# Kernel tuning notes

Measured on AMD Instinct MI355X. Metric: run time of the kernel, lower is better.

Reference implementation:

```python
import jax, jax.numpy as jnp
import numpy as np

S, B, E, H, V, L = 512, 64, 512, 768, 32000, 32
PAD_WORD, PAD_LABEL = 1, 0
PAD_BIAS = 10000.0


def _linear_init(key, fin, fout):
    # matches torch nn.Linear default U(-1/sqrt(fin), 1/sqrt(fin))
    kw, kb = jax.random.split(key)
    s = 1.0 / np.sqrt(fin)
    W = jax.random.uniform(kw, (fin, fout), minval=-s, maxval=s, dtype=jnp.float32)
    b = jax.random.uniform(kb, (fout,), minval=-s, maxval=s, dtype=jnp.float32)
    return W, b


def setup_inputs() -> dict:
    key = jax.random.key(0)
    ks = jax.random.split(key, 9)
    tokens = jax.random.randint(ks[0], (S, B), 0, V, dtype=jnp.int32)
    tags = jax.random.randint(ks[1], (S, B), 0, L, dtype=jnp.int32)
    embedding = jax.random.normal(ks[2], (V, E), dtype=jnp.float32)
    # gate order along the 4H axis: r, f, g, o (matches the 8 separate Linears, stacked)
    Wi_f, bi_f = _linear_init(ks[3], E, 4 * H)
    Wh_f, bh_f = _linear_init(ks[4], H, 4 * H)
    Wi_b, bi_b = _linear_init(ks[5], E, 4 * H)
    Wh_b, bh_b = _linear_init(ks[6], H, 4 * H)
    Wout, bout = _linear_init(ks[7], 2 * H, L)
    return {"tokens": tokens, "tags": tags, "embedding": embedding,
            "Wi_f": Wi_f, "bi_f": bi_f, "Wh_f": Wh_f, "bh_f": bh_f,
            "Wi_b": Wi_b, "bi_b": bi_b, "Wh_b": Wh_b, "bh_b": bh_b,
            "Wout": Wout, "bout": bout}


def _forward(tokens, embedding, Wi_f, bi_f, Wh_f, bh_f, Wi_b, bi_b, Wh_b, bh_b, Wout, bout):
    emb = embedding[tokens]                      # [S,B,E]
    b = tokens.shape[1]
    h = emb.shape[-1] * 0 + Wh_f.shape[0]
    # ---- forward direction: true LSTM-style recurrence ----
    xf = jnp.einsum('sbe,eg->sbg', emb, Wi_f) + bi_f   # [S,B,4H] precomputed input gates

    def step_f(carry, x):
        hid, c = carry
        g = x + hid @ Wh_f + bh_f
        r, f, gg, o = jnp.split(g, 4, axis=-1)
        c = jax.nn.sigmoid(f) * c + jax.nn.sigmoid(r) * jnp.tanh(gg)
        hid = jax.nn.sigmoid(o) * jnp.tanh(c)
        return (hid, c), hid

    z = jnp.zeros((b, h), dtype=emb.dtype)
    (hT, _), hs_f = jax.lax.scan(step_f, (z, z), xf)   # hs_f: [S,B,H]

    # ---- backward direction: source never updates `hidden`, so the hidden
    # projection uses the CONSTANT final forward hidden hT at every step.
    gb = jnp.einsum('sbe,eg->sbg', emb, Wi_b) + bi_b + hT @ Wh_b + bh_b  # [S,B,4H]
    r2, f2, g2, o2 = jnp.split(gb, 4, axis=-1)
    r2 = jax.nn.sigmoid(r2); f2 = jax.nn.sigmoid(f2)
    g2 = jnp.tanh(g2);       o2 = jax.nn.sigmoid(o2)

    def step_b(c2, gates):
        r, f, g, o = gates
        c2 = f * c2 + r * g
        return c2, o * jnp.tanh(c2)

    _, hs_b = jax.lax.scan(step_b, z, (r2, f2, g2, o2), reverse=True)  # [S,B,H], original order

    outputs = jnp.concatenate([hs_f, hs_b], axis=-1)   # [S,B,2H]
    out = outputs @ Wout + bout                        # [S,B,L]
    pad_mask = (tokens == PAD_WORD).astype(out.dtype)
    out = out.at[:, :, PAD_LABEL].add(pad_mask * PAD_BIAS)
    return out


def reference(tokens, tags, embedding, Wi_f, bi_f, Wh_f, bh_f, Wi_b, bi_b, Wh_b, bh_b, Wout, bout):
    del tags  # unused in forward, kept for signature fidelity
    return _forward(tokens, embedding, Wi_f, bi_f, Wh_f, bh_f, Wi_b, bi_b, Wh_b, bh_b, Wout, bout)
```

## Files before the change

kernel.cpp:

```cpp
#include <hip/hip_runtime.h>
#include <hip/hip_bf16.h>
#include <stdint.h>

typedef __attribute__((ext_vector_type(8))) short bf16x8;
typedef __attribute__((ext_vector_type(4))) float f32x4;
typedef __attribute__((ext_vector_type(4))) unsigned int u32x4;
typedef unsigned long long ull_t;

#define S_LEN 512
#define B_DIM 64
#define E_DIM 512
#define H_DIM 768
#define G4    3072
#define H2    1536
#define M_ROWS 32768
#define CHUNK 128
#define CM    8192
#define SLW   24
#define WPS   8
#define WPR   256
#define RWRD  4096
#define PSTR  16384
#define KRES  640
#define KREG  4
#define WROW  648
#define NTILES 1536

__device__ __forceinline__ float sigmf_(float x) { return 1.0f / (1.0f + __expf(-x)); }
__device__ __forceinline__ float tanhf2(float x) {
  x = fminf(fmaxf(x, -20.0f), 20.0f);
  float e = __expf(2.0f * x);
  return (e - 1.0f) / (e + 1.0f);
}
__device__ __forceinline__ float bfu(unsigned short u) { return __uint_as_float((unsigned)u << 16); }
__device__ __forceinline__ unsigned short packbf(float a) {
  __hip_bfloat16 t = __float2bfloat16(a);
  unsigned short b;
  __builtin_memcpy(&b, &t, 2);
  return b;
}

__global__ __launch_bounds__(256) void k_gather(const int* __restrict__ tokens,
                                                const float* __restrict__ emb,
                                                __hip_bfloat16* __restrict__ out) {
  const int t = blockIdx.x * 256 + threadIdx.x;
  const int e0 = t * 8;
  const int row = e0 >> 9;
  const int k = e0 & 511;
  const int tok = tokens[row];
  const float4* p = (const float4*)(emb + (size_t)tok * E_DIM + k);
  const float4 v0 = p[0], v1 = p[1];
  __align__(16) __hip_bfloat16 tmp[8];
  tmp[0] = __float2bfloat16(v0.x); tmp[1] = __float2bfloat16(v0.y);
  tmp[2] = __float2bfloat16(v0.z); tmp[3] = __float2bfloat16(v0.w);
  tmp[4] = __float2bfloat16(v1.x); tmp[5] = __float2bfloat16(v1.y);
  tmp[6] = __float2bfloat16(v1.z); tmp[7] = __float2bfloat16(v1.w);
  *(bf16x8*)(out + (size_t)t * 8) = *(const bf16x8*)tmp;
}

__global__ __launch_bounds__(256) void k_transpose_cast(const float* __restrict__ src,
                                                        __hip_bfloat16* __restrict__ dst,
                                                        int Rs, int Cs) {
  __shared__ float tile[32][33];
  const int tx = threadIdx.x & 31, ty = threadIdx.x >> 5;
  const int c0 = blockIdx.x * 32, r0 = blockIdx.y * 32;
  #pragma unroll
  for (int i = ty; i < 32; i += 8)
    tile[i][tx] = src[(size_t)(r0 + i) * Cs + c0 + tx];
  __syncthreads();
  #pragma unroll
  for (int i = ty; i < 32; i += 8)
    dst[(size_t)(c0 + i) * Rs + r0 + tx] = __float2bfloat16(tile[tx][i]);
}

__global__ __launch_bounds__(256) void k_bias(const float* __restrict__ bi,
                                              const float* __restrict__ bh,
                                              float* __restrict__ bias) {
  const int n = blockIdx.x * 256 + threadIdx.x;
  bias[n] = bi[n] + bh[n];
}

__device__ __forceinline__ void gemm_tile_e(char* pool, int tile,
                                            const __hip_bfloat16* __restrict__ A,
                                            const __hip_bfloat16* __restrict__ BT,
                                            const float* __restrict__ bias,
                                            __hip_bfloat16* __restrict__ C) {
  auto As = (__hip_bfloat16 (*)[40])pool;
  auto Bs = (__hip_bfloat16 (*)[40])(pool + 10240);
  const int tid = threadIdx.x;
  const int wave = tid >> 6, lane = tid & 63;
  const int q = lane >> 4, lr = lane & 15;
  const int wm = (wave >> 1) * 64, wn = (wave & 1) * 64;
  const int nb = tile % 24, mb = tile / 24;
  const int m0 = mb * 128, n0 = nb * 128;
  const int srow = tid >> 2, skseg = (tid & 3) * 8;

  f32x4 acc[4][4];
  #pragma unroll
  for (int i = 0; i < 4; ++i)
    #pragma unroll
    for (int j = 0; j < 4; ++j) { f32x4 z = {0.f, 0.f, 0.f, 0.f}; acc[i][j] = z; }

  for (int kt = 0; kt < 16; ++kt) {
    __syncthreads();
    const int kbase = kt * 32 + skseg;
    *(bf16x8*)&As[srow][skseg]      = *(const bf16x8*)(A + (size_t)(m0 + srow) * E_DIM + kbase);
    *(bf16x8*)&As[srow + 64][skseg] = *(const bf16x8*)(A + (size_t)(m0 + srow + 64) * E_DIM + kbase);
    *(bf16x8*)&Bs[srow][skseg]      = *(const bf16x8*)(BT + (size_t)(n0 + srow) * E_DIM + kbase);
    *(bf16x8*)&Bs[srow + 64][skseg] = *(const bf16x8*)(BT + (size_t)(n0 + srow + 64) * E_DIM + kbase);
    __syncthreads();
    bf16x8 af[4], bfr[4];
    #pragma unroll
    for (int mt = 0; mt < 4; ++mt) af[mt] = *(const bf16x8*)&As[wm + mt * 16 + lr][q * 8];
    #pragma unroll
    for (int nt = 0; nt < 4; ++nt) bfr[nt] = *(const bf16x8*)&Bs[wn + nt * 16 + lr][q * 8];
    #pragma unroll
    for (int mt = 0; mt < 4; ++mt)
      #pragma unroll
      for (int nt = 0; nt < 4; ++nt)
        acc[mt][nt] = __builtin_amdgcn_mfma_f32_16x16x32_bf16(af[mt], bfr[nt], acc[mt][nt], 0, 0, 0);
  }
  #pragma unroll
  for (int mt = 0; mt < 4; ++mt) {
    #pragma unroll
    for (int nt = 0; nt < 4; ++nt) {
      const int col = n0 + wn + nt * 16 + lr;
      const float bv = bias[col];
      #pragma unroll
      for (int i = 0; i < 4; ++i) {
        const int row = m0 + wm + mt * 16 + q * 4 + i;
        C[(size_t)row * G4 + col] = __float2bfloat16(acc[mt][nt][i] + bv);
      }
    }
  }
}

__device__ __forceinline__ void gemm_tile_g(char* pool, int tile,
                                            const int* __restrict__ tokens_c,
                                            const float* __restrict__ emb,
                                            const __hip_bfloat16* __restrict__ BT,
                                            const float* __restrict__ bias,
                                            __hip_bfloat16* __restrict__ C) {
  auto As = (__hip_bfloat16 (*)[40])pool;
  auto Bs = (__hip_bfloat16 (*)[40])(pool + 10240);
  const int tid = threadIdx.x;
  const int wave = tid >> 6, lane = tid & 63;
  const int q = lane >> 4, lr = lane & 15;
  const int wm = (wave >> 1) * 64, wn = (wave & 1) * 64;
  const int nb = tile % 24, mb = tile / 24;
  const int m0 = mb * 128, n0 = nb * 128;
  const int srow = tid >> 2, skseg = (tid & 3) * 8;
  const int tok0 = tokens_c[m0 + srow];
  const int tok1 = tokens_c[m0 + srow + 64];

  f32x4 acc[4][4];
  #pragma unroll
  for (int i = 0; i < 4; ++i)
    #pragma unroll
    for (int j = 0; j < 4; ++j) { f32x4 z = {0.f, 0.f, 0.f, 0.f}; acc[i][j] = z; }

  for (int kt = 0; kt < 16; ++kt) {
    __syncthreads();
    const int kbase = kt * 32 + skseg;
    {
      const float* ap = emb + (size_t)tok0 * E_DIM + kbase;
      const float4 v0 = *(const float4*)ap, v1 = *(const float4*)(ap + 4);
      __align__(16) __hip_bfloat16 t8[8];
      t8[0] = __float2bfloat16(v0.x); t8[1] = __float2bfloat16(v0.y);
      t8[2] = __float2bfloat16(v0.z); t8[3] = __float2bfloat16(v0.w);
      t8[4] = __float2bfloat16(v1.x); t8[5] = __float2bfloat16(v1.y);
      t8[6] = __float2bfloat16(v1.z); t8[7] = __float2bfloat16(v1.w);
      *(bf16x8*)&As[srow][skseg] = *(const bf16x8*)t8;
    }
    {
      const float* ap = emb + (size_t)tok1 * E_DIM + kbase;
      const float4 v0 = *(const float4*)ap, v1 = *(const float4*)(ap + 4);
      __align__(16) __hip_bfloat16 t8[8];
      t8[0] = __float2bfloat16(v0.x); t8[1] = __float2bfloat16(v0.y);
      t8[2] = __float2bfloat16(v0.z); t8[3] = __float2bfloat16(v0.w);
      t8[4] = __float2bfloat16(v1.x); t8[5] = __float2bfloat16(v1.y);
      t8[6] = __float2bfloat16(v1.z); t8[7] = __float2bfloat16(v1.w);
      *(bf16x8*)&As[srow + 64][skseg] = *(const bf16x8*)t8;
    }
    *(bf16x8*)&Bs[srow][skseg]      = *(const bf16x8*)(BT + (size_t)(n0 + srow) * E_DIM + kbase);
    *(bf16x8*)&Bs[srow + 64][skseg] = *(const bf16x8*)(BT + (size_t)(n0 + srow + 64) * E_DIM + kbase);
    __syncthreads();
    bf16x8 af[4], bfr[4];
    #pragma unroll
    for (int mt = 0; mt < 4; ++mt) af[mt] = *(const bf16x8*)&As[wm + mt * 16 + lr][q * 8];
    #pragma unroll
    for (int nt = 0; nt < 4; ++nt) bfr[nt] = *(const bf16x8*)&Bs[wn + nt * 16 + lr][q * 8];
    #pragma unroll
    for (int mt = 0; mt < 4; ++mt)
      #pragma unroll
      for (int nt = 0; nt < 4; ++nt)
        acc[mt][nt] = __builtin_amdgcn_mfma_f32_16x16x32_bf16(af[mt], bfr[nt], acc[mt][nt], 0, 0, 0);
  }
  #pragma unroll
  for (int mt = 0; mt < 4; ++mt) {
    #pragma unroll
    for (int nt = 0; nt < 4; ++nt) {
      const int col = n0 + wn + nt * 16 + lr;
      const float bv = bias[col];
      #pragma unroll
      for (int i = 0; i < 4; ++i) {
        const int row = m0 + wm + mt * 16 + q * 4 + i;
        C[(size_t)row * G4 + col] = __float2bfloat16(acc[mt][nt][i] + bv);
      }
    }
  }
}

__global__ __launch_bounds__(256) void k_gemm_e(const __hip_bfloat16* __restrict__ A,
                                                const __hip_bfloat16* __restrict__ BT,
                                                const float* __restrict__ bias,
                                                __hip_bfloat16* __restrict__ C) {
  __shared__ __align__(16) char pool[20480];
  gemm_tile_e(pool, blockIdx.x, A, BT, bias, C);
}
__global__ __launch_bounds__(256) void k_gemm_g(const int* __restrict__ tokens_c,
                                                const float* __restrict__ emb,
                                                const __hip_bfloat16* __restrict__ BT,
                                                const float* __restrict__ bias,
                                                __hip_bfloat16* __restrict__ C) {
  __shared__ __align__(16) char pool[20480];
  gemm_tile_g(pool, blockIdx.x, tokens_c, emb, BT, bias, C);
}

__device__ __forceinline__ void out_block8(char* pool, int ob,
                                           const __hip_bfloat16* __restrict__ Hs,
                                           const float* __restrict__ Wout,
                                           const float* __restrict__ bout,
                                           const int* __restrict__ tokens,
                                           float* __restrict__ out) {
  auto rowbuf = (float (*)[1536])pool;
  const int r0 = ob * 8;
  const int tid = threadIdx.x;
  for (int idx = tid; idx < 8 * 1536; idx += 256) {
    const int rr = idx / 1536, k = idx % 1536;
    rowbuf[rr][k] = __bfloat162float(Hs[(size_t)(r0 + rr) * H2 + k]);
  }
  __syncthreads();
  const int l = tid & 31, rr = tid >> 5;
  float acc = bout[l];
  #pragma unroll 8
  for (int k = 0; k < 1536; ++k) acc += rowbuf[rr][k] * Wout[k * 32 + l];
  const int row = r0 + rr;
  if (l == 0 && tokens[row] == 1) acc += 10000.0f;
  out[(size_t)row * 32 + l] = acc;
  __syncthreads();
}

__global__ __launch_bounds__(256) void k_out(const __hip_bfloat16* __restrict__ Hs,
                                             const float* __restrict__ Wout,
                                             const float* __restrict__ bout,
                                             const int* __restrict__ tokens,
                                             float* __restrict__ out) {
  __shared__ __align__(16) char pool[49152];
  out_block8(pool, blockIdx.x, Hs, Wout, bout, tokens, out);
}

__global__ __launch_bounds__(256, 1) void k_fwd_fused(const __hip_bfloat16* __restrict__ X,
                                                      const __hip_bfloat16* __restrict__ WhTf,
                                                      ull_t* __restrict__ hbuf,
                                                      __hip_bfloat16* __restrict__ Hs,
                                                      float* __restrict__ cstate,
                                                      float* __restrict__ hT,
                                                      int chunk,
                                                      const __hip_bfloat16* __restrict__ EmbA,
                                                      const int* __restrict__ tokens_nx,
                                                      const float* __restrict__ emb,
                                                      const __hip_bfloat16* __restrict__ WiT_nx,
                                                      const float* __restrict__ Bias_nx,
                                                      __hip_bfloat16* __restrict__ Xw) {
  __shared__ __align__(16) char pool[155904];
  const int bx = blockIdx.x;

  if (bx >= 128) {
    const int nw = gridDim.x - 128;
    if (EmbA) {
      for (int t = bx - 128; t < NTILES; t += nw)
        gemm_tile_e(pool, t, EmbA, WiT_nx, Bias_nx, Xw);
    } else {
      for (int t = bx - 128; t < NTILES; t += nw)
        gemm_tile_g(pool, t, tokens_nx, emb, WiT_nx, Bias_nx, Xw);
    }
    return;
  }

  unsigned short* wlds = (unsigned short*)pool;
  auto h_stage = (unsigned short (*)[776])(pool + 124416);
  auto g_lds   = (float (*)[16][26])(pool + 149248);

  const int group = bx >> 5;
  const int slice = bx & 31;
  const int r0 = group * 16;
  const int j0 = slice * SLW;
  const int tid = threadIdx.x;
  const int w = tid >> 6;
  const int lane = tid & 63;
  const int q = lane >> 4, lr = lane & 15;
  const int base = chunk * CHUNK;

  const int prow = tid >> 4;
  const int pw   = tid & 15;

  const int row  = tid >> 3;
  const int wloc = tid & 7;
  const int col0 = 3 * wloc;

  for (int c = tid; c < 96 * (KRES / 8); c += 256) {
    const int r = c / (KRES / 8), k8 = c % (KRES / 8);
    const int gate = r / SLW, n = r % SLW;
    const float4 v = *(const float4*)(WhTf + (size_t)(gate * H_DIM + j0 + n) * H_DIM + k8 * 8);
    *(float4*)(wlds + (size_t)r * WROW + k8 * 8) = v;
  }

  const int wn0 = lr;
  const int wn1 = 16 + (lr & 7);
  bf16x8 wr0[KREG], wr1[KREG];
  #pragma unroll
  for (int kk = 0; kk < KREG; ++kk) {
    const int ko = KRES + kk * 32 + q * 8;
    wr0[kk] = *(const bf16x8*)(WhTf + (size_t)(w * H_DIM + j0 + wn0) * H_DIM + ko);
    wr1[kk] = *(const bf16x8*)(WhTf + (size_t)(w * H_DIM + j0 + wn1) * H_DIM + ko);
  }

  float cr[3] = {0.f, 0.f, 0.f};
  if (tid < 128) {
    const float* cs = cstate + (size_t)(r0 + row) * H_DIM + j0 + col0;
    cr[0] = cs[0]; cr[1] = cs[1]; cr[2] = cs[2];
  }

  const unsigned skipbit = ((pw >> 2) == (slice & 3)) ? (1u << (slice >> 2)) : 0u;

  __syncthreads();

  for (int s = 0; s < CHUNK; ++s) {
    const int gs = base + s;

    unsigned short xs[4][3];
    if (tid < 128) {
      const unsigned short* xp = (const unsigned short*)(X + ((size_t)s * B_DIM + r0 + row) * G4 + j0 + col0);
      #pragma unroll
      for (int g = 0; g < 4; ++g)
        #pragma unroll
        for (int j = 0; j < 3; ++j) xs[g][j] = xp[g * H_DIM + j];
    }

    const ull_t* hc = hbuf + ((size_t)(gs & 1)) * PSTR + (size_t)group * RWRD
                    + (size_t)prow * WPR + 2 * pw;
    u32x4 d0 = {0,0,0,0}, d1 = {0,0,0,0}, d2 = {0,0,0,0}, d3 = {0,0,0,0};
    u32x4 d4 = {0,0,0,0}, d5 = {0,0,0,0}, d6 = {0,0,0,0}, d7 = {0,0,0,0};
    const unsigned pollmask = (s == 0) ? 0xFFu : (0xFFu ^ skipbit);
    {
      const unsigned e16 = (unsigned)(unsigned short)gs;
      unsigned need = pollmask;
      long guard = 0;
      for (;;) {
#define POLL_LD(i, dv) \
        if (need & (1u << (i))) \
          asm volatile("global_load_dwordx4 %0, %1, off sc0 sc1" \
                       : "=v"(dv) : "v"(hc + 32 * (i)) : "memory");
        POLL_LD(0, d0) POLL_LD(1, d1) POLL_LD(2, d2) POLL_LD(3, d3)
        POLL_LD(4, d4) POLL_LD(5, d5) POLL_LD(6, d6) POLL_LD(7, d7)
#undef POLL_LD
        asm volatile("s_waitcnt vmcnt(0)"
                     : "+v"(d0), "+v"(d1), "+v"(d2), "+v"(d3),
                       "+v"(d4), "+v"(d5), "+v"(d6), "+v"(d7)
                     :: "memory");
        unsigned nn = 0;
#define POLL_CK(i, dv) \
        if ((need & (1u << (i))) && \
            ((((dv).x & 0xFFFFu) != e16) || (((dv).z & 0xFFFFu) != e16))) nn |= 1u << (i);
        POLL_CK(0, d0) POLL_CK(1, d1) POLL_CK(2, d2) POLL_CK(3, d3)
        POLL_CK(4, d4) POLL_CK(5, d5) POLL_CK(6, d6) POLL_CK(7, d7)
#undef POLL_CK
        need = nn;
        if (!need) break;
        if (++guard > (1L << 20)) break;
        __builtin_amdgcn_s_sleep(1);
      }
    }
    {
#define STAGE_PAIR(i, dv) \
      if (pollmask & (1u << (i))) { \
        unsigned* hp = (unsigned*)&h_stage[prow][6 * pw + 96 * (i)]; \
        hp[0] = ((dv).x >> 16) | ((dv).y << 16); \
        hp[1] = ((dv).y >> 16) | ((dv).z & 0xFFFF0000u); \
        hp[2] = (dv).w; \
      }
      STAGE_PAIR(0, d0) STAGE_PAIR(1, d1) STAGE_PAIR(2, d2) STAGE_PAIR(3, d3)
      STAGE_PAIR(4, d4) STAGE_PAIR(5, d5) STAGE_PAIR(6, d6) STAGE_PAIR(7, d7)
#undef STAGE_PAIR
    }
    __syncthreads();

    f32x4 acc0 = {0.f, 0.f, 0.f, 0.f};
    f32x4 acc1 = {0.f, 0.f, 0.f, 0.f};
    {
      const unsigned short* wb = wlds + (size_t)w * SLW * WROW;
      #pragma unroll
      for (int kt = 0; kt < KRES / 32; ++kt) {
        const int ko = kt * 32 + q * 8;
        const bf16x8 a  = *(const bf16x8*)&h_stage[lr][ko];
        const bf16x8 b0 = *(const bf16x8*)(wb + (size_t)wn0 * WROW + ko);
        const bf16x8 b1 = *(const bf16x8*)(wb + (size_t)wn1 * WROW + ko);
        acc0 = __builtin_amdgcn_mfma_f32_16x16x32_bf16(a, b0, acc0, 0, 0, 0);
        acc1 = __builtin_amdgcn_mfma_f32_16x16x32_bf16(a, b1, acc1, 0, 0, 0);
      }
      #pragma unroll
      for (int kk = 0; kk < KREG; ++kk) {
        const bf16x8 a = *(const bf16x8*)&h_stage[lr][KRES + kk * 32 + q * 8];
        acc0 = __builtin_amdgcn_mfma_f32_16x16x32_bf16(a, wr0[kk], acc0, 0, 0, 0);
        acc1 = __builtin_amdgcn_mfma_f32_16x16x32_bf16(a, wr1[kk], acc1, 0, 0, 0);
      }
    }
    #pragma unroll
    for (int i = 0; i < 4; ++i) g_lds[w][q * 4 + i][lr] = acc0[i];
    if (lr < 8) {
      #pragma unroll
      for (int i = 0; i < 4; ++i) g_lds[w][q * 4 + i][16 + lr] = acc1[i];
    }
    __syncthreads();

    if (tid < 128) {
      float h[3];
      #pragma unroll
      for (int j = 0; j < 3; ++j) {
        const float rv = g_lds[0][row][col0 + j] + bfu(xs[0][j]);
        const float fv = g_lds[1][row][col0 + j] + bfu(xs[1][j]);
        const float gv = g_lds[2][row][col0 + j] + bfu(xs[2][j]);
        const float ov = g_lds[3][row][col0 + j] + bfu(xs[3][j]);
        const float c = sigmf_(fv) * cr[j] + sigmf_(rv) * tanhf2(gv);
        cr[j] = c;
        h[j] = sigmf_(ov) * tanhf2(c);
      }
      const unsigned short b0 = packbf(h[0]), b1 = packbf(h[1]), b2 = packbf(h[2]);
      const ull_t wv = (ull_t)(unsigned short)(gs + 1)
                     | ((ull_t)b0 << 16) | ((ull_t)b1 << 32) | ((ull_t)b2 << 48);
      __hip_atomic_store(hbuf + ((size_t)((gs + 1) & 1)) * PSTR + (size_t)group * RWRD
                         + (size_t)row * WPR + slice * WPS + wloc,
                         wv, __ATOMIC_RELAXED, __HIP_MEMORY_SCOPE_AGENT);
      h_stage[row][j0 + col0]     = b0;
      h_stage[row][j0 + col0 + 1] = b1;
      h_stage[row][j0 + col0 + 2] = b2;
      unsigned short* hsp = (unsigned short*)(Hs + ((size_t)gs * B_DIM + r0 + row) * H2 + j0 + col0);
      hsp[0] = b0; hsp[1] = b1; hsp[2] = b2;
      if (chunk == 3 && s == CHUNK - 1) {
        float* hp = hT + (size_t)(r0 + row) * H_DIM + j0 + col0;
        hp[0] = h[0]; hp[1] = h[1]; hp[2] = h[2];
      }
    }
  }

  if (tid < 128) {
    float* cs = cstate + (size_t)(r0 + row) * H_DIM + j0 + col0;
    cs[0] = cr[0]; cs[1] = cr[1]; cs[2] = cr[2];
  }
}

__global__ __launch_bounds__(256) void k_hTW(const float* __restrict__ hT,
                                             const float* __restrict__ Whb,
                                             float* __restrict__ hTW) {
  const int b = blockIdx.y;
  const int n = blockIdx.x * 256 + threadIdx.x;
  __shared__ float hs[768];
  for (int i = threadIdx.x; i < 768; i += 256) hs[i] = hT[b * 768 + i];
  __syncthreads();
  float acc = 0.f;
  #pragma unroll 4
  for (int k = 0; k < 768; ++k) acc += hs[k] * Whb[(size_t)k * G4 + n];
  hTW[(size_t)b * G4 + n] = acc;
}

__global__ __launch_bounds__(256) void k_bwd_scan_o(const __hip_bfloat16* __restrict__ X,
                                                    const float* __restrict__ hTW,
                                                    __hip_bfloat16* __restrict__ Hs,
                                                    float* __restrict__ c2state,
                                                    int chunk,
                                                    const __hip_bfloat16* __restrict__ EmbB,
                                                    const __hip_bfloat16* __restrict__ WiTb,
                                                    const float* __restrict__ BiasB,
                                                    __hip_bfloat16* __restrict__ Xw,
                                                    int do_gemm, int out_chunk,
                                                    const float* __restrict__ Wout,
                                                    const float* __restrict__ bout,
                                                    const int* __restrict__ tokens,
                                                    float* __restrict__ out) {
  __shared__ __align__(16) char pool[49152];
  const int bx = blockIdx.x;

  if (bx >= 448) {
    if (out_chunk >= 0)
      for (int ob = bx - 448; ob < 1024; ob += 128)
        out_block8(pool, out_chunk * 1024 + ob, Hs, Wout, bout, tokens, out);
    return;
  }
  if (bx >= 192) {
    if (do_gemm)
      for (int t = bx - 192; t < NTILES; t += 256)
        gemm_tile_e(pool, t, EmbB, WiTb, BiasB, Xw);
    return;
  }

  const int t = bx * 256 + threadIdx.x;
  const int b = t / H_DIM;
  const int j = t % H_DIM;
  const int base = chunk * CHUNK;
  const float hw0 = hTW[(size_t)b * G4 + j];
  const float hw1 = hTW[(size_t)b * G4 + 768 + j];
  const float hw2 = hTW[(size_t)b * G4 + 1536 + j];
  const float hw3 = hTW[(size_t)b * G4 + 2304 + j];
  float c2 = c2state[t];
  for (int s = CHUNK - 1; s >= 0; --s) {
    const size_t xb = ((size_t)s * B_DIM + b) * G4 + j;
    const float r = sigmf_(__bfloat162float(X[xb]) + hw0);
    const float f = sigmf_(__bfloat162float(X[xb + 768]) + hw1);
    const float g = tanhf2(__bfloat162float(X[xb + 1536]) + hw2);
    const float o = sigmf_(__bfloat162float(X[xb + 2304]) + hw3);
    c2 = f * c2 + r * g;
    Hs[((size_t)(base + s) * B_DIM + b) * H2 + H_DIM + j] = __float2bfloat16(o * tanhf2(c2));
  }
  c2state[t] = c2;
}

extern "C" void kernel_launch(void* const* d_in, const int* in_sizes, int n_in,
                              void* d_out, int out_size, void* d_ws, size_t ws_size,
                              hipStream_t stream) {
  const int*   tokens = (const int*)d_in[0];
  const float* emb    = (const float*)d_in[2];
  const float* Wi_f   = (const float*)d_in[3];
  const float* bi_f   = (const float*)d_in[4];
  const float* Wh_f   = (const float*)d_in[5];
  const float* bh_f   = (const float*)d_in[6];
  const float* Wi_b   = (const float*)d_in[7];
  const float* bi_b   = (const float*)d_in[8];
  const float* Wh_b   = (const float*)d_in[9];
  const float* bh_b   = (const float*)d_in[10];
  const float* Wout   = (const float*)d_in[11];
  const float* bout   = (const float*)d_in[12];
  float* out = (float*)d_out;
  char* ws = (char*)d_ws;

  size_t off = 0;
  auto alloc = [&](size_t bytes) { size_t o = off; off += (bytes + 255) & ~(size_t)255; return o; };
  const size_t oHs    = alloc((size_t)M_ROWS * H2 * 2);
  const size_t oX0    = alloc((size_t)CM * G4 * 2);
  const size_t oWhTf  = alloc((size_t)G4 * H_DIM * 2);
  const size_t oWiTf  = alloc((size_t)G4 * E_DIM * 2);
  const size_t oWiTb  = alloc((size_t)G4 * E_DIM * 2);
  const size_t oBiasF = alloc((size_t)G4 * 4);
  const size_t oBiasB = alloc((size_t)G4 * 4);
  const size_t oHbuf  = alloc((size_t)2 * PSTR * 8);
  const size_t oCst   = alloc((size_t)B_DIM * H_DIM * 4);
  const size_t oHT    = alloc((size_t)B_DIM * H_DIM * 4);
  const size_t oHTW   = alloc((size_t)B_DIM * G4 * 4);
  const size_t oC2    = alloc((size_t)B_DIM * H_DIM * 4);
  const size_t oX1    = alloc((size_t)CM * G4 * 2);
  const bool overlap = (off <= ws_size);
  const size_t oEmb   = alloc((size_t)M_ROWS * E_DIM * 2);
  const bool tierA = (off <= ws_size);
  (void)in_sizes; (void)n_in; (void)out_size;

  __hip_bfloat16* Hs   = (__hip_bfloat16*)(ws + oHs);
  __hip_bfloat16* X0   = (__hip_bfloat16*)(ws + oX0);
  __hip_bfloat16* X1   = overlap ? (__hip_bfloat16*)(ws + oX1) : X0;
  __hip_bfloat16* Emb  = tierA ? (__hip_bfloat16*)(ws + oEmb) : (__hip_bfloat16*)nullptr;
  __hip_bfloat16* WhTf = (__hip_bfloat16*)(ws + oWhTf);
  __hip_bfloat16* WiTf = (__hip_bfloat16*)(ws + oWiTf);
  __hip_bfloat16* WiTb = (__hip_bfloat16*)(ws + oWiTb);
  float*          BiasF= (float*)(ws + oBiasF);
  float*          BiasB= (float*)(ws + oBiasB);
  ull_t*          Hbuf = (ull_t*)(ws + oHbuf);
  float*          Cst  = (float*)(ws + oCst);
  float*          HT   = (float*)(ws + oHT);
  float*          HTW  = (float*)(ws + oHTW);
  float*          C2   = (float*)(ws + oC2);

  hipMemsetAsync(ws + oHbuf, 0, (size_t)2 * PSTR * 8, stream);
  hipMemsetAsync(ws + oCst, 0, (size_t)B_DIM * H_DIM * 4, stream);
  hipMemsetAsync(ws + oC2, 0, (size_t)B_DIM * H_DIM * 4, stream);

  if (tierA)
    k_gather<<<8192, 256, 0, stream>>>(tokens, emb, Emb);
  k_transpose_cast<<<dim3(96, 24), 256, 0, stream>>>(Wh_f, WhTf, 768, 3072);
  k_transpose_cast<<<dim3(96, 16), 256, 0, stream>>>(Wi_f, WiTf, 512, 3072);
  k_transpose_cast<<<dim3(96, 16), 256, 0, stream>>>(Wi_b, WiTb, 512, 3072);
  k_bias<<<12, 256, 0, stream>>>(bi_f, bh_f, BiasF);
  k_bias<<<12, 256, 0, stream>>>(bi_b, bh_b, BiasB);

  auto EA = [&](int c) { return Emb + (size_t)c * CM * E_DIM; };

  if (tierA) {
    k_gemm_e<<<NTILES, 256, 0, stream>>>(Emb, WiTf, BiasF, X0);
    k_fwd_fused<<<240, 256, 0, stream>>>(X0, WhTf, Hbuf, Hs, Cst, HT, 0,
                                         EA(1), tokens, emb, WiTf, BiasF, X1);
    k_fwd_fused<<<240, 256, 0, stream>>>(X1, WhTf, Hbuf, Hs, Cst, HT, 1,
                                         EA(2), tokens, emb, WiTf, BiasF, X0);
    k_fwd_fused<<<240, 256, 0, stream>>>(X0, WhTf, Hbuf, Hs, Cst, HT, 2,
                                         EA(3), tokens, emb, WiTf, BiasF, X1);
    k_fwd_fused<<<240, 256, 0, stream>>>(X1, WhTf, Hbuf, Hs, Cst, HT, 3,
                                         EA(3), tokens, emb, WiTb, BiasB, X0);
    k_hTW<<<dim3(12, 64), 256, 0, stream>>>(HT, Wh_b, HTW);
    k_bwd_scan_o<<<576, 256, 0, stream>>>(X0, HTW, Hs, C2, 3,
                                          EA(2), WiTb, BiasB, X1, 1, -1,
                                          Wout, bout, tokens, out);
    k_bwd_scan_o<<<576, 256, 0, stream>>>(X1, HTW, Hs, C2, 2,
                                          EA(1), WiTb, BiasB, X0, 1, 3,
                                          Wout, bout, tokens, out);
    k_bwd_scan_o<<<576, 256, 0, stream>>>(X0, HTW, Hs, C2, 1,
                                          EA(0), WiTb, BiasB, X1, 1, 2,
                                          Wout, bout, tokens, out);
    k_bwd_scan_o<<<576, 256, 0, stream>>>(X1, HTW, Hs, C2, 0,
                                          nullptr, WiTb, BiasB, X0, 0, 1,
                                          Wout, bout, tokens, out);
    k_out<<<1024, 256, 0, stream>>>(Hs, Wout, bout, tokens, out);
  } else if (overlap) {
    k_gemm_g<<<NTILES, 256, 0, stream>>>(tokens, emb, WiTf, BiasF, X0);
    k_fwd_fused<<<240, 256, 0, stream>>>(X0, WhTf, Hbuf, Hs, Cst, HT, 0,
                                         nullptr, tokens + 1 * CM, emb, WiTf, BiasF, X1);
    k_fwd_fused<<<240, 256, 0, stream>>>(X1, WhTf, Hbuf, Hs, Cst, HT, 1,
                                         nullptr, tokens + 2 * CM, emb, WiTf, BiasF, X0);
    k_fwd_fused<<<240, 256, 0, stream>>>(X0, WhTf, Hbuf, Hs, Cst, HT, 2,
                                         nullptr, tokens + 3 * CM, emb, WiTf, BiasF, X1);
    k_fwd_fused<<<240, 256, 0, stream>>>(X1, WhTf, Hbuf, Hs, Cst, HT, 3,
                                         nullptr, tokens + 3 * CM, emb, WiTb, BiasB, X0);
    k_hTW<<<dim3(12, 64), 256, 0, stream>>>(HT, Wh_b, HTW);
    k_bwd_scan_o<<<192, 256, 0, stream>>>(X0, HTW, Hs, C2, 3,
                                          nullptr, WiTb, BiasB, X1, 0, -1,
                                          Wout, bout, tokens, out);
    for (int c = 2; c >= 0; --c) {
      k_gemm_g<<<NTILES, 256, 0, stream>>>(tokens + (size_t)c * CM, emb, WiTb, BiasB, X1);
      k_bwd_scan_o<<<192, 256, 0, stream>>>(X1, HTW, Hs, C2, c,
                                            nullptr, WiTb, BiasB, X0, 0, -1,
                                            Wout, bout, tokens, out);
    }
    k_out<<<4096, 256, 0, stream>>>(Hs, Wout, bout, tokens, out);
  } else {
    for (int c = 0; c < 4; ++c) {
      k_gemm_g<<<NTILES, 256, 0, stream>>>(tokens + (size_t)c * CM, emb, WiTf, BiasF, X0);
      k_fwd_fused<<<128, 256, 0, stream>>>(X0, WhTf, Hbuf, Hs, Cst, HT, c,
                                           nullptr, tokens, emb, WiTf, BiasF, X0);
    }
    k_hTW<<<dim3(12, 64), 256, 0, stream>>>(HT, Wh_b, HTW);
    for (int c = 3; c >= 0; --c) {
      k_gemm_g<<<NTILES, 256, 0, stream>>>(tokens + (size_t)c * CM, emb, WiTb, BiasB, X0);
      k_bwd_scan_o<<<192, 256, 0, stream>>>(X0, HTW, Hs, C2, c,
                                            nullptr, WiTb, BiasB, X0, 0, -1,
                                            Wout, bout, tokens, out);
    }
    k_out<<<4096, 256, 0, stream>>>(Hs, Wout, bout, tokens, out);
  }
}
```

Baseline: 3.332 ms.

## Merge prep kernels; split backward scan from overlapped GEMM and output work

Combines the embedding gather, three weight transpose-casts and two bias adds into one k_prep launch to cut launch overhead. In the tierA path it also stops overlapping the backward scan with the next chunk's input GEMM and the output projection inside one kernel. Those become separate serial launches of k_bwd_scan, k_gemm_e and one full k_out at the end. This trades the overlap of the latency-bound scan with GEMM and output work for simpler kernels, which may lose concurrency.

```diff
diff --git a/kernel.cpp b/kernel.cpp
--- a/kernel.cpp
+++ b/kernel.cpp
@@ -40,30 +40,12 @@
   return b;
 }
 
-__global__ __launch_bounds__(256) void k_gather(const int* __restrict__ tokens,
-                                                const float* __restrict__ emb,
-                                                __hip_bfloat16* __restrict__ out) {
-  const int t = blockIdx.x * 256 + threadIdx.x;
-  const int e0 = t * 8;
-  const int row = e0 >> 9;
-  const int k = e0 & 511;
-  const int tok = tokens[row];
-  const float4* p = (const float4*)(emb + (size_t)tok * E_DIM + k);
-  const float4 v0 = p[0], v1 = p[1];
-  __align__(16) __hip_bfloat16 tmp[8];
-  tmp[0] = __float2bfloat16(v0.x); tmp[1] = __float2bfloat16(v0.y);
-  tmp[2] = __float2bfloat16(v0.z); tmp[3] = __float2bfloat16(v0.w);
-  tmp[4] = __float2bfloat16(v1.x); tmp[5] = __float2bfloat16(v1.y);
-  tmp[6] = __float2bfloat16(v1.z); tmp[7] = __float2bfloat16(v1.w);
-  *(bf16x8*)(out + (size_t)t * 8) = *(const bf16x8*)tmp;
-}
-
-__global__ __launch_bounds__(256) void k_transpose_cast(const float* __restrict__ src,
-                                                        __hip_bfloat16* __restrict__ dst,
-                                                        int Rs, int Cs) {
-  __shared__ float tile[32][33];
+__device__ __forceinline__ void transpose_body(float (*tile)[33],
+                                               const float* __restrict__ src,
+                                               __hip_bfloat16* __restrict__ dst,
+                                               int Rs, int Cs, int bxx, int bxy) {
   const int tx = threadIdx.x & 31, ty = threadIdx.x >> 5;
-  const int c0 = blockIdx.x * 32, r0 = blockIdx.y * 32;
+  const int c0 = bxx * 32, r0 = bxy * 32;
   #pragma unroll
   for (int i = ty; i < 32; i += 8)
     tile[i][tx] = src[(size_t)(r0 + i) * Cs + c0 + tx];
@@ -73,11 +55,46 @@
     dst[(size_t)(c0 + i) * Rs + r0 + tx] = __float2bfloat16(tile[tx][i]);
 }
 
-__global__ __launch_bounds__(256) void k_bias(const float* __restrict__ bi,
-                                              const float* __restrict__ bh,
-                                              float* __restrict__ bias) {
-  const int n = blockIdx.x * 256 + threadIdx.x;
-  bias[n] = bi[n] + bh[n];
+__global__ __launch_bounds__(256) void k_prep(const int* __restrict__ tokens,
+                                              const float* __restrict__ emb,
+                                              __hip_bfloat16* __restrict__ Emb,
+                                              const float* __restrict__ Wh_f, __hip_bfloat16* __restrict__ WhTf,
+                                              const float* __restrict__ Wi_f, __hip_bfloat16* __restrict__ WiTf,
+                                              const float* __restrict__ Wi_b, __hip_bfloat16* __restrict__ WiTb,
+                                              const float* __restrict__ bi_f, const float* __restrict__ bh_f,
+                                              float* __restrict__ BiasF,
+                                              const float* __restrict__ bi_b, const float* __restrict__ bh_b,
+                                              float* __restrict__ BiasB) {
+  __shared__ float tile[32][33];
+  int bx = blockIdx.x;
+  if (bx < 8192) {
+    if (Emb) {
+      const int t = bx * 256 + threadIdx.x;
+      const int e0 = t * 8;
+      const int row = e0 >> 9;
+      const int k = e0 & 511;
+      const int tok = tokens[row];
+      const float4* p = (const float4*)(emb + (size_t)tok * E_DIM + k);
+      const float4 v0 = p[0], v1 = p[1];
+      __align__(16) __hip_bfloat16 tmp[8];
+      tmp[0] = __float2bfloat16(v0.x); tmp[1] = __float2bfloat16(v0.y);
+      tmp[2] = __float2bfloat16(v0.z); tmp[3] = __float2bfloat16(v0.w);
+      tmp[4] = __float2bfloat16(v1.x); tmp[5] = __float2bfloat16(v1.y);
+      tmp[6] = __float2bfloat16(v1.z); tmp[7] = __float2bfloat16(v1.w);
+      *(bf16x8*)(Emb + (size_t)t * 8) = *(const bf16x8*)tmp;
+    }
+    return;
+  }
+  bx -= 8192;
+  if (bx < 2304) { transpose_body(tile, Wh_f, WhTf, 768, 3072, bx % 96, bx / 96); return; }
+  bx -= 2304;
+  if (bx < 1536) { transpose_body(tile, Wi_f, WiTf, 512, 3072, bx % 96, bx / 96); return; }
+  bx -= 1536;
+  if (bx < 1536) { transpose_body(tile, Wi_b, WiTb, 512, 3072, bx % 96, bx / 96); return; }
+  bx -= 1536;
+  if (bx < 12) { const int n = bx * 256 + threadIdx.x; BiasF[n] = bi_f[n] + bh_f[n]; return; }
+  bx -= 12;
+  { const int n = bx * 256 + threadIdx.x; BiasB[n] = bi_b[n] + bh_b[n]; }
 }
 
 __device__ __forceinline__ void gemm_tile_e(char* pool, int tile,
@@ -227,14 +244,13 @@
   gemm_tile_g(pool, blockIdx.x, tokens_c, emb, BT, bias, C);
 }
 
-__device__ __forceinline__ void out_block8(char* pool, int ob,
-                                           const __hip_bfloat16* __restrict__ Hs,
-                                           const float* __restrict__ Wout,
-                                           const float* __restrict__ bout,
-                                           const int* __restrict__ tokens,
-                                           float* __restrict__ out) {
-  auto rowbuf = (float (*)[1536])pool;
-  const int r0 = ob * 8;
+__global__ __launch_bounds__(256) void k_out(const __hip_bfloat16* __restrict__ Hs,
+                                             const float* __restrict__ Wout,
+                                             const float* __restrict__ bout,
+                                             const int* __restrict__ tokens,
+                                             float* __restrict__ out) {
+  __shared__ float rowbuf[8][1536];
+  const int r0 = blockIdx.x * 8;
   const int tid = threadIdx.x;
   for (int idx = tid; idx < 8 * 1536; idx += 256) {
     const int rr = idx / 1536, k = idx % 1536;
@@ -248,16 +264,6 @@
   const int row = r0 + rr;
   if (l == 0 && tokens[row] == 1) acc += 10000.0f;
   out[(size_t)row * 32 + l] = acc;
-  __syncthreads();
-}
-
-__global__ __launch_bounds__(256) void k_out(const __hip_bfloat16* __restrict__ Hs,
-                                             const float* __restrict__ Wout,
-                                             const float* __restrict__ bout,
-                                             const int* __restrict__ tokens,
-                                             float* __restrict__ out) {
-  __shared__ __align__(16) char pool[49152];
-  out_block8(pool, blockIdx.x, Hs, Wout, bout, tokens, out);
 }
 
 __global__ __launch_bounds__(256, 1) void k_fwd_fused(const __hip_bfloat16* __restrict__ X,
@@ -474,37 +480,12 @@
   hTW[(size_t)b * G4 + n] = acc;
 }
 
-__global__ __launch_bounds__(256) void k_bwd_scan_o(const __hip_bfloat16* __restrict__ X,
-                                                    const float* __restrict__ hTW,
-                                                    __hip_bfloat16* __restrict__ Hs,
-                                                    float* __restrict__ c2state,
-                                                    int chunk,
-                                                    const __hip_bfloat16* __restrict__ EmbB,
-                                                    const __hip_bfloat16* __restrict__ WiTb,
-                                                    const float* __restrict__ BiasB,
-                                                    __hip_bfloat16* __restrict__ Xw,
-                                                    int do_gemm, int out_chunk,
-                                                    const float* __restrict__ Wout,
-                                                    const float* __restrict__ bout,
-                                                    const int* __restrict__ tokens,
-                                                    float* __restrict__ out) {
-  __shared__ __align__(16) char pool[49152];
-  const int bx = blockIdx.x;
-
-  if (bx >= 448) {
-    if (out_chunk >= 0)
-      for (int ob = bx - 448; ob < 1024; ob += 128)
-        out_block8(pool, out_chunk * 1024 + ob, Hs, Wout, bout, tokens, out);
-    return;
-  }
-  if (bx >= 192) {
-    if (do_gemm)
-      for (int t = bx - 192; t < NTILES; t += 256)
-        gemm_tile_e(pool, t, EmbB, WiTb, BiasB, Xw);
-    return;
-  }
-
-  const int t = bx * 256 + threadIdx.x;
+__global__ __launch_bounds__(256) void k_bwd_scan(const __hip_bfloat16* __restrict__ X,
+                                                  const float* __restrict__ hTW,
+                                                  __hip_bfloat16* __restrict__ Hs,
+                                                  float* __restrict__ c2state,
+                                                  int chunk) {
+  const int t = blockIdx.x * 256 + threadIdx.x;
   const int b = t / H_DIM;
   const int j = t % H_DIM;
   const int base = chunk * CHUNK;
@@ -582,13 +563,9 @@
   hipMemsetAsync(ws + oCst, 0, (size_t)B_DIM * H_DIM * 4, stream);
   hipMemsetAsync(ws + oC2, 0, (size_t)B_DIM * H_DIM * 4, stream);
 
-  if (tierA)
-    k_gather<<<8192, 256, 0, stream>>>(tokens, emb, Emb);
-  k_transpose_cast<<<dim3(96, 24), 256, 0, stream>>>(Wh_f, WhTf, 768, 3072);
-  k_transpose_cast<<<dim3(96, 16), 256, 0, stream>>>(Wi_f, WiTf, 512, 3072);
-  k_transpose_cast<<<dim3(96, 16), 256, 0, stream>>>(Wi_b, WiTb, 512, 3072);
-  k_bias<<<12, 256, 0, stream>>>(bi_f, bh_f, BiasF);
-  k_bias<<<12, 256, 0, stream>>>(bi_b, bh_b, BiasB);
+  k_prep<<<13592, 256, 0, stream>>>(tokens, emb, Emb,
+                                    Wh_f, WhTf, Wi_f, WiTf, Wi_b, WiTb,
+                                    bi_f, bh_f, BiasF, bi_b, bh_b, BiasB);
 
   auto EA = [&](int c) { return Emb + (size_t)c * CM * E_DIM; };
 
@@ -603,19 +580,14 @@
     k_fwd_fused<<<240, 256, 0, stream>>>(X1, WhTf, Hbuf, Hs, Cst, HT, 3,
                                          EA(3), tokens, emb, WiTb, BiasB, X0);
     k_hTW<<<dim3(12, 64), 256, 0, stream>>>(HT, Wh_b, HTW);
-    k_bwd_scan_o<<<576, 256, 0, stream>>>(X0, HTW, Hs, C2, 3,
-                                          EA(2), WiTb, BiasB, X1, 1, -1,
-                                          Wout, bout, tokens, out);
-    k_bwd_scan_o<<<576, 256, 0, stream>>>(X1, HTW, Hs, C2, 2,
-                                          EA(1), WiTb, BiasB, X0, 1, 3,
-                                          Wout, bout, tokens, out);
-    k_bwd_scan_o<<<576, 256, 0, stream>>>(X0, HTW, Hs, C2, 1,
-                                          EA(0), WiTb, BiasB, X1, 1, 2,
-                                          Wout, bout, tokens, out);
-    k_bwd_scan_o<<<576, 256, 0, stream>>>(X1, HTW, Hs, C2, 0,
-                                          nullptr, WiTb, BiasB, X0, 0, 1,
-                                          Wout, bout, tokens, out);
-    k_out<<<1024, 256, 0, stream>>>(Hs, Wout, bout, tokens, out);
+    k_bwd_scan<<<192, 256, 0, stream>>>(X0, HTW, Hs, C2, 3);
+    k_gemm_e<<<NTILES, 256, 0, stream>>>(EA(2), WiTb, BiasB, X1);
+    k_bwd_scan<<<192, 256, 0, stream>>>(X1, HTW, Hs, C2, 2);
+    k_gemm_e<<<NTILES, 256, 0, stream>>>(EA(1), WiTb, BiasB, X0);
+    k_bwd_scan<<<192, 256, 0, stream>>>(X0, HTW, Hs, C2, 1);
+    k_gemm_e<<<NTILES, 256, 0, stream>>>(EA(0), WiTb, BiasB, X1);
+    k_bwd_scan<<<192, 256, 0, stream>>>(X1, HTW, Hs, C2, 0);
+    k_out<<<4096, 256, 0, stream>>>(Hs, Wout, bout, tokens, out);
   } else if (overlap) {
     k_gemm_g<<<NTILES, 256, 0, stream>>>(tokens, emb, WiTf, BiasF, X0);
     k_fwd_fused<<<240, 256, 0, stream>>>(X0, WhTf, Hbuf, Hs, Cst, HT, 0,
@@ -627,14 +599,10 @@
     k_fwd_fused<<<240, 256, 0, stream>>>(X1, WhTf, Hbuf, Hs, Cst, HT, 3,
                                          nullptr, tokens + 3 * CM, emb, WiTb, BiasB, X0);
     k_hTW<<<dim3(12, 64), 256, 0, stream>>>(HT, Wh_b, HTW);
-    k_bwd_scan_o<<<192, 256, 0, stream>>>(X0, HTW, Hs, C2, 3,
-                                          nullptr, WiTb, BiasB, X1, 0, -1,
-                                          Wout, bout, tokens, out);
+    k_bwd_scan<<<192, 256, 0, stream>>>(X0, HTW, Hs, C2, 3);
     for (int c = 2; c >= 0; --c) {
       k_gemm_g<<<NTILES, 256, 0, stream>>>(tokens + (size_t)c * CM, emb, WiTb, BiasB, X1);
-      k_bwd_scan_o<<<192, 256, 0, stream>>>(X1, HTW, Hs, C2, c,
-                                            nullptr, WiTb, BiasB, X0, 0, -1,
-                                            Wout, bout, tokens, out);
+      k_bwd_scan<<<192, 256, 0, stream>>>(X1, HTW, Hs, C2, c);
     }
     k_out<<<4096, 256, 0, stream>>>(Hs, Wout, bout, tokens, out);
   } else {
@@ -646,9 +614,7 @@
     k_hTW<<<dim3(12, 64), 256, 0, stream>>>(HT, Wh_b, HTW);
     for (int c = 3; c >= 0; --c) {
       k_gemm_g<<<NTILES, 256, 0, stream>>>(tokens + (size_t)c * CM, emb, WiTb, BiasB, X0);
-      k_bwd_scan_o<<<192, 256, 0, stream>>>(X0, HTW, Hs, C2, c,
-                                            nullptr, WiTb, BiasB, X0, 0, -1,
-                                            Wout, bout, tokens, out);
+      k_bwd_scan<<<192, 256, 0, stream>>>(X0, HTW, Hs, C2, c);
     }
     k_out<<<4096, 256, 0, stream>>>(Hs, Wout, bout, tokens, out);
   }
```

Result: faster. 2.969 ms (-10.9%).
